# Kernel tuning notes

Measured on AMD Instinct MI355X. Metric: run time of the kernel, lower is better.

The kernel has to match this reference:

```python
import jax, jax.numpy as jnp
import numpy as np

B, S, E, H = 2, 2048, 2048, 16
D = E // H  # head_dim = 128


def _rope_tables(seq_len, dim):
    # standard RoPE: theta_i = 10000^(-2i/dim), angles duplicated over pair halves
    inv_freq = 1.0 / (10000.0 ** (np.arange(0, dim, 2, dtype=np.float32) / dim))
    angles = np.arange(seq_len, dtype=np.float32)[:, None] * inv_freq[None, :]  # [S, D/2]
    angles = np.concatenate([angles, angles], axis=-1)  # [S, D]
    return jnp.asarray(np.cos(angles)), jnp.asarray(np.sin(angles))


def setup_inputs() -> dict:
    key = jax.random.key(0)
    ks = jax.random.split(key, 10)
    sc = 1.0 / np.sqrt(E)
    cos, sin = _rope_tables(S, D)
    mask = jnp.tril(jnp.ones((S, S), dtype=bool))[None, None]  # causal [1,1,S,S]
    return {
        "x_q": jax.random.normal(ks[0], (B, S, E), jnp.float32),
        "x_kv": jax.random.normal(ks[1], (B, S, E), jnp.float32),
        "cos": cos,
        "sin": sin,
        "wq": jax.random.normal(ks[2], (E, E), jnp.float32) * sc,
        "bq": jax.random.normal(ks[3], (E,), jnp.float32) * 0.01,
        "wk": jax.random.normal(ks[4], (E, E), jnp.float32) * sc,
        "bk": jax.random.normal(ks[5], (E,), jnp.float32) * 0.01,
        "wv": jax.random.normal(ks[6], (E, E), jnp.float32) * sc,
        "bv": jax.random.normal(ks[7], (E,), jnp.float32) * 0.01,
        "wo": jax.random.normal(ks[8], (E, E), jnp.float32) * sc,
        "bo": jax.random.normal(ks[9], (E,), jnp.float32) * 0.01,
        "mask": mask,
    }


def _apply_rope(x, cos, sin):
    # x: [B,H,S,D]; cos/sin: [S,D]. rotate-half convention.
    x1, x2 = jnp.split(x, 2, axis=-1)
    rot = jnp.concatenate([-x2, x1], axis=-1)
    return x * cos[None, None] + rot * sin[None, None]


def reference(x_q, x_kv, cos, sin, wq, bq, wk, bk, wv, bv, wo, bo, mask):
    b, sq, _ = x_q.shape
    skv = x_kv.shape[1]
    q = (x_q @ wq.T + bq).reshape(b, sq, H, D).transpose(0, 2, 1, 3)   # [B,H,Sq,D]
    k = (x_kv @ wk.T + bk).reshape(b, skv, H, D).transpose(0, 2, 1, 3)
    v = (x_kv @ wv.T + bv).reshape(b, skv, H, D).transpose(0, 2, 1, 3)
    q = _apply_rope(q, cos, sin)
    k = _apply_rope(k, cos, sin)
    scores = jnp.einsum("bhqd,bhkd->bhqk", q, k) / jnp.sqrt(jnp.float32(D))
    scores = jnp.where(mask, scores, jnp.float32(-1e9))
    w = jax.nn.softmax(scores, axis=-1)  # dropout p=0 -> identity
    out = jnp.einsum("bhqk,bhkd->bhqd", w, v)
    out = out.transpose(0, 2, 1, 3).reshape(b, sq, H * D)
    return out @ wo.T + bo
```

## Files before the change

### kernel.cpp

```cpp
#include <hip/hip_runtime.h>
#include <hip/hip_bf16.h>

#define Bb 2
#define Ss 2048
#define Ee 2048
#define Hh 16
#define Dd 128
#define Mrows (Bb*Ss)

typedef short short8 __attribute__((ext_vector_type(8)));
typedef float f32x4 __attribute__((ext_vector_type(4)));

__device__ __forceinline__ unsigned short bf_rne(float f) {
    unsigned u = __builtin_bit_cast(unsigned, f);
    u += 0x7fffu + ((u >> 16) & 1u);
    return (unsigned short)(u >> 16);
}
__device__ __forceinline__ float bf2f(unsigned short x) {
    unsigned u = ((unsigned)x) << 16;
    return __builtin_bit_cast(float, u);
}
__device__ __forceinline__ void load_lds16(const void* g, void* l) {
    __builtin_amdgcn_global_load_lds(
        (const __attribute__((address_space(1))) unsigned int*)g,
        (__attribute__((address_space(3))) unsigned int*)l, 16, 0, 0);
}

__global__ void cast_all_kernel(const float4* __restrict__ xq, const float4* __restrict__ xkv,
                                const float4* __restrict__ wq, const float4* __restrict__ wk,
                                const float4* __restrict__ wv, const float4* __restrict__ wo,
                                ushort4* __restrict__ out) {
    int i = blockIdx.x * 256 + threadIdx.x;
    const float4* src;
    int rel;
    if (i < 2097152)       { src = xq;  rel = i; }
    else if (i < 4194304)  { src = xkv; rel = i - 2097152; }
    else if (i < 5242880)  { src = wq;  rel = i - 4194304; }
    else if (i < 6291456)  { src = wk;  rel = i - 5242880; }
    else if (i < 7340032)  { src = wv;  rel = i - 6291456; }
    else                   { src = wo;  rel = i - 7340032; }
    float4 v = src[rel];
    ushort4 o;
    o.x = bf_rne(v.x); o.y = bf_rne(v.y); o.z = bf_rne(v.z); o.w = bf_rne(v.w);
    out[i] = o;
}

__device__ __forceinline__ void gemm_core(
    const short* __restrict__ A, const short* __restrict__ W, int K,
    int m0, int n0, int wave, int lane, short* As, short* Bs, f32x4 acc[4][4])
{
    const int wm = (wave & 1) * 64;
    const int wn = (wave >> 1) * 64;
    const int quad = lane >> 4;
    const int l16  = lane & 15;
    const int lrow   = lane >> 3;
    const int gchunk = (lane & 7) ^ lrow;

    for (int kt = 0; kt < K; kt += 64) {
        __syncthreads();
        #pragma unroll
        for (int j = 0; j < 4; ++j) {
            int row = wave*32 + j*8 + lrow;
            load_lds16(A + (size_t)(m0 + row)*K + kt + gchunk*8, &As[(wave*32 + j*8)*64]);
            load_lds16(W + (size_t)(n0 + row)*K + kt + gchunk*8, &Bs[(wave*32 + j*8)*64]);
        }
        __syncthreads();

        #pragma unroll
        for (int ks = 0; ks < 64; ks += 32) {
            const int cs = ks >> 3;
            short8 af[4], bfr[4];
            #pragma unroll
            for (int i = 0; i < 4; ++i)
                af[i] = *(const short8*)&As[(wm + i*16 + l16)*64 + (((cs + quad) ^ (l16 & 7)) << 3)];
            #pragma unroll
            for (int j = 0; j < 4; ++j)
                bfr[j] = *(const short8*)&Bs[(wn + j*16 + l16)*64 + (((cs + quad) ^ (l16 & 7)) << 3)];
            #pragma unroll
            for (int i = 0; i < 4; ++i)
                #pragma unroll
                for (int j = 0; j < 4; ++j)
                    acc[i][j] = __builtin_amdgcn_mfma_f32_16x16x32_bf16(af[i], bfr[j], acc[i][j], 0, 0, 0);
        }
    }
}

union GemmSmem {
    struct { short As[128*64]; short Bs[128*64]; } st;
    short T[128*137];
};

__global__ __launch_bounds__(256) void qkv_gemm(
    const short* __restrict__ xq, const short* __restrict__ xkv,
    const short* __restrict__ wq, const short* __restrict__ wk, const short* __restrict__ wv,
    const float* __restrict__ bq, const float* __restrict__ bk, const float* __restrict__ bv,
    short* __restrict__ Qr, short* __restrict__ Kr, short* __restrict__ VT)
{
    __shared__ GemmSmem sm;
    const int tid  = threadIdx.x;
    const int wave = tid >> 6;
    const int lane = tid & 63;
    const int quad = lane >> 4;
    const int l16  = lane & 15;
    const int m0   = blockIdx.x * 128;
    const int sub  = blockIdx.y >> 4;
    const int nb   = blockIdx.y & 15;
    const int n0   = nb * 128;
    const int wm = (wave & 1) * 64;
    const int wn = (wave >> 1) * 64;

    const short* A = (sub == 0) ? xq : xkv;
    const short* W = (sub == 0) ? wq : (sub == 1) ? wk : wv;
    const float* bias = (sub == 0) ? bq : (sub == 1) ? bk : bv;

    f32x4 acc[4][4] = {};
    gemm_core(A, W, Ee, m0, n0, wave, lane, sm.st.As, sm.st.Bs, acc);

    const int b0 = m0 >> 11;
    const int s0 = m0 & (Ss - 1);

    if (sub < 2) {
        short* out = (sub == 0) ? Qr : Kr;
        #pragma unroll
        for (int i = 0; i < 4; ++i)
            #pragma unroll
            for (int j = 0; j < 4; ++j)
                #pragma unroll
                for (int r = 0; r < 4; ++r) {
                    int gm = m0 + wm + i*16 + quad*4 + r;
                    int gn = n0 + wn + j*16 + l16;
                    float v = acc[i][j][r] + bias[gn];
                    int b = gm >> 11, s = gm & (Ss-1);
                    int h = gn >> 7,  d = gn & (Dd-1);
                    out[(((size_t)(b*Hh + h)) * Ss + s) * Dd + d] = (short)bf_rne(v);
                }
    } else {
        __syncthreads();
        #pragma unroll
        for (int i = 0; i < 4; ++i)
            #pragma unroll
            for (int j = 0; j < 4; ++j)
                #pragma unroll
                for (int r = 0; r < 4; ++r) {
                    int ml = wm + i*16 + quad*4 + r;
                    int nl = wn + j*16 + l16;
                    sm.T[ml*137 + nl] = (short)bf_rne(acc[i][j][r] + bias[n0 + nl]);
                }
        __syncthreads();
        const int g = tid & 15, dbase = tid >> 4;
        const int h = nb;
        #pragma unroll
        for (int dd = 0; dd < 8; ++dd) {
            int d = dbase + dd*16;
            short8 v;
            #pragma unroll
            for (int c = 0; c < 8; ++c)
                v[c] = sm.T[(g*8 + c)*137 + d];
            *(short8*)&VT[(((size_t)(b0*Hh + h)) * Dd + d) * Ss + s0 + g*8] = v;
        }
    }
}

__global__ __launch_bounds__(256) void oproj_gemm(
    const short* __restrict__ A, const short* __restrict__ W,
    const float* __restrict__ bias, float* __restrict__ Cf)
{
    __shared__ GemmSmem sm;
    const int tid  = threadIdx.x;
    const int wave = tid >> 6;
    const int lane = tid & 63;
    const int quad = lane >> 4;
    const int l16  = lane & 15;
    const int m0 = blockIdx.x * 128;
    const int n0 = blockIdx.y * 128;
    const int wm = (wave & 1) * 64;
    const int wn = (wave >> 1) * 64;

    f32x4 acc[4][4] = {};
    gemm_core(A, W, Ee, m0, n0, wave, lane, sm.st.As, sm.st.Bs, acc);

    #pragma unroll
    for (int i = 0; i < 4; ++i)
        #pragma unroll
        for (int j = 0; j < 4; ++j)
            #pragma unroll
            for (int r = 0; r < 4; ++r) {
                int gm = m0 + wm + i*16 + quad*4 + r;
                int gn = n0 + wn + j*16 + l16;
                Cf[(size_t)gm * Ee + gn] = acc[i][j][r] + bias[gn];
            }
}

__global__ void rope_kernel(short* __restrict__ Qr, short* __restrict__ Kr,
                            const float* __restrict__ cosT, const float* __restrict__ sinT) {
    short* X    = blockIdx.y ? Kr : Qr;
    float scale = blockIdx.y ? 1.0f : 0.08838834764831845f;
    int idx = blockIdx.x * 256 + threadIdx.x;
    int d  = idx & 63;
    int s  = (idx >> 6) & (Ss - 1);
    int bh = idx >> 17;
    size_t base = ((size_t)bh * Ss + s) * Dd;
    float x1 = bf2f((unsigned short)X[base + d]);
    float x2 = bf2f((unsigned short)X[base + d + 64]);
    float c  = cosT[s*Dd + d];
    float sn = sinT[s*Dd + d];
    X[base + d]      = (short)bf_rne((x1 * c - x2 * sn) * scale);
    X[base + d + 64] = (short)bf_rne((x2 * c + x1 * sn) * scale);
}

__global__ __launch_bounds__(256, 2) void attn_kernel(
    const short* __restrict__ Q, const short* __restrict__ Kk,
    const short* __restrict__ VT, short* __restrict__ O)
{
    __shared__ short Ks[64*128];
    __shared__ short Vt[2][128*64];
    __shared__ short Pw[4][32*72];

    const int tid  = threadIdx.x;
    const int wave = tid >> 6;
    const int lane = tid & 63;
    const int quad = lane >> 4;
    const int l16  = lane & 15;
    const int mmap = (blockIdx.x + blockIdx.y) & 15;
    const int qt   = (blockIdx.y & 16) ? (15 - mmap) : mmap;
    const int bh = blockIdx.y;
    const int b  = bh >> 4, h = bh & 15;
    const size_t head_off = (size_t)bh * Ss * Dd;
    const short* Kg  = Kk + head_off;
    const short* VTg = VT + head_off;

    auto stageK = [&](int kt) {
        #pragma unroll
        for (int j = 0; j < 4; ++j) {
            int r = wave*16 + j*4 + (lane >> 4);
            int c = (lane & 15) ^ (r & 15);
            load_lds16(Kg + (size_t)(kt*64 + r)*Dd + c*8, &Ks[(wave*16 + j*4)*128]);
        }
    };
    auto stageV = [&](int kt, int buf) {
        #pragma unroll
        for (int j = 0; j < 4; ++j) {
            int r = wave*32 + j*8 + (lane >> 3);
            int c = (lane & 7) ^ (r & 7);
            load_lds16(VTg + (size_t)r*Ss + kt*64 + c*8, &Vt[buf][(wave*32 + j*8)*64]);
        }
    };

    const int qbase = qt*128 + wave*32;
    short8 qf[2][4];
    #pragma unroll
    for (int mi = 0; mi < 2; ++mi)
        #pragma unroll
        for (int ds = 0; ds < 4; ++ds)
            qf[mi][ds] = *(const short8*)&Q[head_off + (size_t)(qbase + mi*16 + l16)*Dd + ds*32 + quad*8];

    f32x4 o[2][8] = {};
    float m_i[2][4], l_i[2][4];
    #pragma unroll
    for (int mi = 0; mi < 2; ++mi)
        #pragma unroll
        for (int r = 0; r < 4; ++r) { m_i[mi][r] = -__builtin_inff(); l_i[mi][r] = 0.f; }

    const int ktiles = 2*qt + 2;
    stageK(0);
    stageV(0, 0);

    for (int kt = 0; kt < ktiles; ++kt) {
        __syncthreads();
        if (kt + 1 < ktiles) stageV(kt+1, (kt+1)&1);

        f32x4 sc[2][4] = {};
        #pragma unroll
        for (int jk = 0; jk < 4; ++jk)
            #pragma unroll
            for (int ds = 0; ds < 4; ++ds) {
                short8 kf = *(const short8*)&Ks[(jk*16 + l16)*128 + (((ds*4 + quad) ^ l16) * 8)];
                #pragma unroll
                for (int mi = 0; mi < 2; ++mi)
                    sc[mi][jk] = __builtin_amdgcn_mfma_f32_16x16x32_bf16(qf[mi][ds], kf, sc[mi][jk], 0, 0, 0);
            }

        __syncthreads();
        if (kt + 1 < ktiles) stageK(kt+1);

        const int k0 = kt*64;
        #pragma unroll
        for (int mi = 0; mi < 2; ++mi) {
            if (k0 + 63 > qbase + mi*16) {
                #pragma unroll
                for (int jk = 0; jk < 4; ++jk) {
                    int kg = k0 + jk*16 + l16;
                    #pragma unroll
                    for (int r = 0; r < 4; ++r)
                        if (kg > qbase + mi*16 + quad*4 + r) sc[mi][jk][r] = -__builtin_inff();
                }
            }
        }

        float alpha[2][4];
        #pragma unroll
        for (int mi = 0; mi < 2; ++mi)
            #pragma unroll
            for (int r = 0; r < 4; ++r) {
                float mx = fmaxf(fmaxf(sc[mi][0][r], sc[mi][1][r]), fmaxf(sc[mi][2][r], sc[mi][3][r]));
                #pragma unroll
                for (int off = 1; off < 16; off <<= 1)
                    mx = fmaxf(mx, __shfl_xor(mx, off));
                float mn = fmaxf(m_i[mi][r], mx);
                alpha[mi][r] = __expf(m_i[mi][r] - mn);
                m_i[mi][r] = mn;
                float s = 0.f;
                #pragma unroll
                for (int jk = 0; jk < 4; ++jk) {
                    float p = __expf(sc[mi][jk][r] - mn);
                    sc[mi][jk][r] = p;
                    s += p;
                }
                l_i[mi][r] = l_i[mi][r] * alpha[mi][r] + s;
            }

        #pragma unroll
        for (int mi = 0; mi < 2; ++mi)
            #pragma unroll
            for (int jk = 0; jk < 4; ++jk)
                #pragma unroll
                for (int r = 0; r < 4; ++r)
                    Pw[wave][(mi*16 + quad*4 + r)*72 + jk*16 + l16] = (short)bf_rne(sc[mi][jk][r]);

        #pragma unroll
        for (int mi = 0; mi < 2; ++mi)
            #pragma unroll
            for (int dt = 0; dt < 8; ++dt)
                #pragma unroll
                for (int r = 0; r < 4; ++r)
                    o[mi][dt][r] *= alpha[mi][r];

        short8 pa[2][2];
        #pragma unroll
        for (int mi = 0; mi < 2; ++mi)
            #pragma unroll
            for (int kk = 0; kk < 2; ++kk)
                pa[mi][kk] = *(const short8*)&Pw[wave][(mi*16 + l16)*72 + kk*32 + quad*8];

        const short* vb = Vt[kt & 1];
        #pragma unroll
        for (int dt = 0; dt < 8; ++dt)
            #pragma unroll
            for (int kk = 0; kk < 2; ++kk) {
                short8 vf = *(const short8*)&vb[(dt*16 + l16)*64 + (((kk*4 + quad) ^ (l16 & 7)) * 8)];
                #pragma unroll
                for (int mi = 0; mi < 2; ++mi)
                    o[mi][dt] = __builtin_amdgcn_mfma_f32_16x16x32_bf16(pa[mi][kk], vf, o[mi][dt], 0, 0, 0);
            }
    }

    #pragma unroll
    for (int mi = 0; mi < 2; ++mi)
        #pragma unroll
        for (int r = 0; r < 4; ++r) {
            float l = l_i[mi][r];
            #pragma unroll
            for (int off = 1; off < 16; off <<= 1)
                l += __shfl_xor(l, off);
            float inv = 1.0f / l;
            int srow = qbase + mi*16 + quad*4 + r;
            size_t obase = ((size_t)b * Ss + srow) * Ee + h * Dd;
            #pragma unroll
            for (int dt = 0; dt < 8; ++dt)
                O[obase + dt*16 + l16] = (short)bf_rne(o[mi][dt][r] * inv);
        }
}

extern "C" void kernel_launch(void* const* d_in, const int* in_sizes, int n_in,
                              void* d_out, int out_size, void* d_ws, size_t ws_size,
                              hipStream_t stream) {
    const float* x_q  = (const float*)d_in[0];
    const float* x_kv = (const float*)d_in[1];
    const float* cosT = (const float*)d_in[2];
    const float* sinT = (const float*)d_in[3];
    const float* wq = (const float*)d_in[4];
    const float* bq = (const float*)d_in[5];
    const float* wk = (const float*)d_in[6];
    const float* bk = (const float*)d_in[7];
    const float* wv = (const float*)d_in[8];
    const float* bv = (const float*)d_in[9];
    const float* wo = (const float*)d_in[10];
    const float* bo = (const float*)d_in[11];

    size_t off = 0;
    auto alloc = [&](size_t bytes) {
        void* p = (char*)d_ws + off;
        off += (bytes + 255) & ~(size_t)255;
        return p;
    };
    const size_t nX = (size_t)Mrows * Ee;
    const size_t nW = (size_t)Ee * Ee;
    short* xq16  = (short*)alloc(nX * 2);
    short* xkv16 = (short*)alloc(nX * 2);
    short* wq16  = (short*)alloc(nW * 2);
    short* wk16  = (short*)alloc(nW * 2);
    short* wv16  = (short*)alloc(nW * 2);
    short* wo16  = (short*)alloc(nW * 2);
    short* Qr    = (short*)alloc(nX * 2);
    short* Kr    = (short*)alloc(nX * 2);
    short* VTb   = (short*)alloc(nX * 2);
    short* Ob    = (short*)alloc(nX * 2);

    cast_all_kernel<<<32768, 256, 0, stream>>>(
        (const float4*)x_q, (const float4*)x_kv, (const float4*)wq,
        (const float4*)wk, (const float4*)wv, (const float4*)wo, (ushort4*)xq16);

    qkv_gemm<<<dim3(Mrows/128, 48), 256, 0, stream>>>(
        xq16, xkv16, wq16, wk16, wv16, bq, bk, bv, Qr, Kr, VTb);

    rope_kernel<<<dim3((Bb*Hh*Ss*64)/256, 2), 256, 0, stream>>>(Qr, Kr, cosT, sinT);

    attn_kernel<<<dim3(16, Bb*Hh), 256, 0, stream>>>(Qr, Kr, VTb, Ob);

    oproj_gemm<<<dim3(Mrows/128, Ee/128), 256, 0, stream>>>(Ob, wo16, bo, (float*)d_out);
}
```

Baseline: 458.4 us.

## Compute transposed S^T tiles in attention, passing P through registers instead of LDS

Swaps the MFMA operands so each lane holds scores for a query column (S^T = K·Q^T). Row max and sum then need only two cross-lane shuffles, and the P operand for the PV MFMA is built with register shuffles, which removes the per-wave Pw LDS staging buffer. The rope scale now folds in log2(e) so softmax can use the native exp2 instruction. Output is written as short4 vectors. Dropping Pw reduces LDS use, so launch bounds are raised to 3 blocks per CU, at the cost of extra shuffle instructions and more register pressure.

```diff
diff --git a/kernel.cpp b/kernel.cpp
--- a/kernel.cpp
+++ b/kernel.cpp
@@ -19,6 +19,9 @@
 __device__ __forceinline__ float bf2f(unsigned short x) {
     unsigned u = ((unsigned)x) << 16;
     return __builtin_bit_cast(float, u);
+}
+__device__ __forceinline__ unsigned pack_bf2(float a, float b) {
+    return (unsigned)bf_rne(a) | ((unsigned)bf_rne(b) << 16);
 }
 __device__ __forceinline__ void load_lds16(const void* g, void* l) {
     __builtin_amdgcn_global_load_lds(
@@ -194,7 +197,7 @@
 __global__ void rope_kernel(short* __restrict__ Qr, short* __restrict__ Kr,
                             const float* __restrict__ cosT, const float* __restrict__ sinT) {
     short* X    = blockIdx.y ? Kr : Qr;
-    float scale = blockIdx.y ? 1.0f : 0.08838834764831845f;
+    float scale = blockIdx.y ? 1.0f : 0.1275174253055484f;
     int idx = blockIdx.x * 256 + threadIdx.x;
     int d  = idx & 63;
     int s  = (idx >> 6) & (Ss - 1);
@@ -208,13 +211,12 @@
     X[base + d + 64] = (short)bf_rne((x2 * c + x1 * sn) * scale);
 }
 
-__global__ __launch_bounds__(256, 2) void attn_kernel(
+__global__ __launch_bounds__(256, 3) void attn_kernel(
     const short* __restrict__ Q, const short* __restrict__ Kk,
     const short* __restrict__ VT, short* __restrict__ O)
 {
     __shared__ short Ks[64*128];
     __shared__ short Vt[2][128*64];
-    __shared__ short Pw[4][32*72];
 
     const int tid  = threadIdx.x;
     const int wave = tid >> 6;
@@ -246,20 +248,17 @@
         }
     };
 
-    const int qbase = qt*128 + wave*32;
-    short8 qf[2][4];
+    const int qw = qt*128 + wave*32;
+    short8 qb[2][4];
     #pragma unroll
-    for (int mi = 0; mi < 2; ++mi)
+    for (int qf = 0; qf < 2; ++qf)
         #pragma unroll
         for (int ds = 0; ds < 4; ++ds)
-            qf[mi][ds] = *(const short8*)&Q[head_off + (size_t)(qbase + mi*16 + l16)*Dd + ds*32 + quad*8];
-
-    f32x4 o[2][8] = {};
-    float m_i[2][4], l_i[2][4];
-    #pragma unroll
-    for (int mi = 0; mi < 2; ++mi)
-        #pragma unroll
-        for (int r = 0; r < 4; ++r) { m_i[mi][r] = -__builtin_inff(); l_i[mi][r] = 0.f; }
+            qb[qf][ds] = *(const short8*)&Q[head_off + (size_t)(qw + qf*16 + l16)*Dd + ds*32 + quad*8];
+
+    f32x4 o[8][2] = {};
+    float m_i[2] = {-__builtin_inff(), -__builtin_inff()};
+    float l_i[2] = {0.f, 0.f};
 
     const int ktiles = 2*qt + 2;
     stageK(0);
@@ -269,106 +268,128 @@
         __syncthreads();
         if (kt + 1 < ktiles) stageV(kt+1, (kt+1)&1);
 
-        f32x4 sc[2][4] = {};
-        #pragma unroll
-        for (int jk = 0; jk < 4; ++jk)
+        f32x4 sc[4][2] = {};
+        #pragma unroll
+        for (int kf = 0; kf < 4; ++kf)
             #pragma unroll
             for (int ds = 0; ds < 4; ++ds) {
-                short8 kf = *(const short8*)&Ks[(jk*16 + l16)*128 + (((ds*4 + quad) ^ l16) * 8)];
-                #pragma unroll
-                for (int mi = 0; mi < 2; ++mi)
-                    sc[mi][jk] = __builtin_amdgcn_mfma_f32_16x16x32_bf16(qf[mi][ds], kf, sc[mi][jk], 0, 0, 0);
+                short8 af = *(const short8*)&Ks[(kf*16 + l16)*128 + (((ds*4 + quad) ^ l16) * 8)];
+                #pragma unroll
+                for (int qf = 0; qf < 2; ++qf)
+                    sc[kf][qf] = __builtin_amdgcn_mfma_f32_16x16x32_bf16(af, qb[qf][ds], sc[kf][qf], 0, 0, 0);
             }
 
         __syncthreads();
         if (kt + 1 < ktiles) stageK(kt+1);
 
         const int k0 = kt*64;
-        #pragma unroll
-        for (int mi = 0; mi < 2; ++mi) {
-            if (k0 + 63 > qbase + mi*16) {
-                #pragma unroll
-                for (int jk = 0; jk < 4; ++jk) {
-                    int kg = k0 + jk*16 + l16;
+        if (k0 + 63 > qw) {
+            #pragma unroll
+            for (int kf = 0; kf < 4; ++kf)
+                #pragma unroll
+                for (int qf = 0; qf < 2; ++qf) {
+                    int kg = k0 + kf*16 + quad*4;
+                    int qg = qw + qf*16 + l16;
                     #pragma unroll
                     for (int r = 0; r < 4; ++r)
-                        if (kg > qbase + mi*16 + quad*4 + r) sc[mi][jk][r] = -__builtin_inff();
+                        if (kg + r > qg) sc[kf][qf][r] = -__builtin_inff();
                 }
-            }
-        }
-
-        float alpha[2][4];
-        #pragma unroll
-        for (int mi = 0; mi < 2; ++mi)
-            #pragma unroll
-            for (int r = 0; r < 4; ++r) {
-                float mx = fmaxf(fmaxf(sc[mi][0][r], sc[mi][1][r]), fmaxf(sc[mi][2][r], sc[mi][3][r]));
-                #pragma unroll
-                for (int off = 1; off < 16; off <<= 1)
-                    mx = fmaxf(mx, __shfl_xor(mx, off));
-                float mn = fmaxf(m_i[mi][r], mx);
-                alpha[mi][r] = __expf(m_i[mi][r] - mn);
-                m_i[mi][r] = mn;
-                float s = 0.f;
-                #pragma unroll
-                for (int jk = 0; jk < 4; ++jk) {
-                    float p = __expf(sc[mi][jk][r] - mn);
-                    sc[mi][jk][r] = p;
+        }
+
+        float alpha[2];
+        #pragma unroll
+        for (int qf = 0; qf < 2; ++qf) {
+            float mx = -__builtin_inff();
+            #pragma unroll
+            for (int kf = 0; kf < 4; ++kf)
+                #pragma unroll
+                for (int r = 0; r < 4; ++r)
+                    mx = fmaxf(mx, sc[kf][qf][r]);
+            mx = fmaxf(mx, __shfl_xor(mx, 16));
+            mx = fmaxf(mx, __shfl_xor(mx, 32));
+            float mn = fmaxf(m_i[qf], mx);
+            alpha[qf] = __builtin_amdgcn_exp2f(m_i[qf] - mn);
+            m_i[qf] = mn;
+            float s = 0.f;
+            #pragma unroll
+            for (int kf = 0; kf < 4; ++kf)
+                #pragma unroll
+                for (int r = 0; r < 4; ++r) {
+                    float p = __builtin_amdgcn_exp2f(sc[kf][qf][r] - mn);
+                    sc[kf][qf][r] = p;
                     s += p;
                 }
-                l_i[mi][r] = l_i[mi][r] * alpha[mi][r] + s;
+            l_i[qf] = l_i[qf] * alpha[qf] + s;
+        }
+
+        unsigned pk[4][2][2];
+        #pragma unroll
+        for (int kf = 0; kf < 4; ++kf)
+            #pragma unroll
+            for (int qf = 0; qf < 2; ++qf) {
+                pk[kf][qf][0] = pack_bf2(sc[kf][qf][0], sc[kf][qf][1]);
+                pk[kf][qf][1] = pack_bf2(sc[kf][qf][2], sc[kf][qf][3]);
             }
 
         #pragma unroll
-        for (int mi = 0; mi < 2; ++mi)
-            #pragma unroll
-            for (int jk = 0; jk < 4; ++jk)
+        for (int dt = 0; dt < 8; ++dt)
+            #pragma unroll
+            for (int qf = 0; qf < 2; ++qf)
                 #pragma unroll
                 for (int r = 0; r < 4; ++r)
-                    Pw[wave][(mi*16 + quad*4 + r)*72 + jk*16 + l16] = (short)bf_rne(sc[mi][jk][r]);
-
-        #pragma unroll
-        for (int mi = 0; mi < 2; ++mi)
-            #pragma unroll
-            for (int dt = 0; dt < 8; ++dt)
-                #pragma unroll
-                for (int r = 0; r < 4; ++r)
-                    o[mi][dt][r] *= alpha[mi][r];
-
-        short8 pa[2][2];
-        #pragma unroll
-        for (int mi = 0; mi < 2; ++mi)
-            #pragma unroll
-            for (int kk = 0; kk < 2; ++kk)
-                pa[mi][kk] = *(const short8*)&Pw[wave][(mi*16 + l16)*72 + kk*32 + quad*8];
+                    o[dt][qf][r] *= alpha[qf];
 
         const short* vb = Vt[kt & 1];
-        #pragma unroll
-        for (int dt = 0; dt < 8; ++dt)
-            #pragma unroll
-            for (int kk = 0; kk < 2; ++kk) {
+        const int src0 = ((quad & 1) * 2) * 16 + l16;
+        const int src1 = src0 + 16;
+        #pragma unroll
+        for (int kk = 0; kk < 2; ++kk) {
+            short8 pb[2];
+            #pragma unroll
+            for (int qf = 0; qf < 2; ++qf) {
+                unsigned a0 = __shfl((int)pk[kk*2][qf][0],   src0);
+                unsigned a1 = __shfl((int)pk[kk*2][qf][1],   src0);
+                unsigned a2 = __shfl((int)pk[kk*2][qf][0],   src1);
+                unsigned a3 = __shfl((int)pk[kk*2][qf][1],   src1);
+                unsigned b0 = __shfl((int)pk[kk*2+1][qf][0], src0);
+                unsigned b1 = __shfl((int)pk[kk*2+1][qf][1], src0);
+                unsigned b2 = __shfl((int)pk[kk*2+1][qf][0], src1);
+                unsigned b3 = __shfl((int)pk[kk*2+1][qf][1], src1);
+                uint4 dw;
+                dw.x = (quad < 2) ? a0 : b0;
+                dw.y = (quad < 2) ? a1 : b1;
+                dw.z = (quad < 2) ? a2 : b2;
+                dw.w = (quad < 2) ? a3 : b3;
+                pb[qf] = __builtin_bit_cast(short8, dw);
+            }
+            #pragma unroll
+            for (int dt = 0; dt < 8; ++dt) {
                 short8 vf = *(const short8*)&vb[(dt*16 + l16)*64 + (((kk*4 + quad) ^ (l16 & 7)) * 8)];
                 #pragma unroll
-                for (int mi = 0; mi < 2; ++mi)
-                    o[mi][dt] = __builtin_amdgcn_mfma_f32_16x16x32_bf16(pa[mi][kk], vf, o[mi][dt], 0, 0, 0);
+                for (int qf = 0; qf < 2; ++qf)
+                    o[dt][qf] = __builtin_amdgcn_mfma_f32_16x16x32_bf16(vf, pb[qf], o[dt][qf], 0, 0, 0);
             }
+        }
     }
 
     #pragma unroll
-    for (int mi = 0; mi < 2; ++mi)
-        #pragma unroll
-        for (int r = 0; r < 4; ++r) {
-            float l = l_i[mi][r];
-            #pragma unroll
-            for (int off = 1; off < 16; off <<= 1)
-                l += __shfl_xor(l, off);
-            float inv = 1.0f / l;
-            int srow = qbase + mi*16 + quad*4 + r;
-            size_t obase = ((size_t)b * Ss + srow) * Ee + h * Dd;
-            #pragma unroll
-            for (int dt = 0; dt < 8; ++dt)
-                O[obase + dt*16 + l16] = (short)bf_rne(o[mi][dt][r] * inv);
-        }
+    for (int qf = 0; qf < 2; ++qf) {
+        float l = l_i[qf];
+        l += __shfl_xor(l, 16);
+        l += __shfl_xor(l, 32);
+        float inv = 1.0f / l;
+        int q = qw + qf*16 + l16;
+        size_t obase = ((size_t)b * Ss + q) * Ee + h * Dd + quad*4;
+        #pragma unroll
+        for (int dt = 0; dt < 8; ++dt) {
+            short4 v;
+            v.x = (short)bf_rne(o[dt][qf][0] * inv);
+            v.y = (short)bf_rne(o[dt][qf][1] * inv);
+            v.z = (short)bf_rne(o[dt][qf][2] * inv);
+            v.w = (short)bf_rne(o[dt][qf][3] * inv);
+            *(short4*)&O[obase + dt*16] = v;
+        }
+    }
 }
 
 extern "C" void kernel_launch(void* const* d_in, const int* in_sizes, int n_in,
```

Measured after the change: 513.2 us. 1.12x slower.
